# Performance work log

Hardware: AMD Instinct MI355X
Metric: run time of the kernel (lower is better)

## Reference

```python
import jax, jax.numpy as jnp
import numpy as np

NORM_S = 3.0  # normalize_scale, learn_scale=False
NUM_CLASSES = 32


def setup_inputs() -> dict:
    key = jax.random.key(0)
    k1, k2 = jax.random.split(key)
    x = jax.random.normal(k1, (512, 128), dtype=jnp.float32)
    labels = jax.random.randint(k2, (512,), 0, NUM_CLASSES, dtype=jnp.int64)
    return {"x": x, "labels": labels}


def reference(x, labels):
    # L2-normalize rows and scale (MyTripletLoss.forward)
    f = NORM_S * x / jnp.linalg.norm(x, axis=1, keepdims=True)
    # pairwise squared distances, clamped at 0 (pairwise_distances)
    sq = jnp.sum(f * f, axis=1)
    D = jnp.clip(sq[:, None] + sq[None, :] - 2.0 * (f @ f.T), 0.0, None)  # [N,N]
    N = x.shape[0]
    # triplet_type == 0: valid triplet (i,j,k) iff i!=j, l_i==l_j, l_i!=l_k
    same = (labels[:, None] == labels[None, :]) & (~jnp.eye(N, dtype=bool))  # [i,j]
    diff = labels[:, None] != labels[None, :]                                # [i,k]
    mask = same[:, :, None] & diff[:, None, :]                               # [i,j,k]
    # DBL loss: log(1 + exp(D_ij - D_ik)) = softplus
    lt = jax.nn.softplus(D[:, :, None] - D[:, None, :])                      # [i,j,k]
    triplet_count = jnp.sum(mask).astype(lt.dtype)
    loss = jnp.sum(jnp.where(mask, lt, 0.0)) / triplet_count
    return loss.reshape(1)
```

## Files before the change

kernel.cpp:

```cpp
#include <hip/hip_runtime.h>
#include <math.h>

#define N 512
#define DIM 128
#define NORM_S 3.0f
#define TR 64
#define PADS 132


__global__ void __launch_bounds__(64) normalize_kernel(const float* __restrict__ x,
                                                       float* __restrict__ f) {
    int row = blockIdx.x;
    int lane = threadIdx.x;
    const float2* xr = (const float2*)(x + row * DIM);
    float2 v = xr[lane];
    float s = v.x * v.x + v.y * v.y;
    #pragma unroll
    for (int off = 32; off > 0; off >>= 1) s += __shfl_xor(s, off, 64);
    float scale = NORM_S / sqrtf(s);
    float2 fv;
    fv.x = v.x * scale;
    fv.y = v.y * scale;
    ((float2*)(f + row * DIM))[lane] = fv;
}

__global__ void __launch_bounds__(256) triplet_kernel(const float* __restrict__ f,
                                                      const int* __restrict__ labels,
                                                      float* __restrict__ sums,
                                                      float* __restrict__ cnts) {
    __shared__ float xt[TR * PADS];
    __shared__ float xi[DIM];
    __shared__ int   lab[N];
    __shared__ float sameD[N];
    __shared__ float diffD[N];
    __shared__ float part[256];
    __shared__ float red[256];
    __shared__ int   nsame, ndiff;

    int i = blockIdx.x;
    int t = threadIdx.x;

    if (t < DIM) xi[t] = f[i * DIM + t];
    for (int j = t; j < N; j += 256) lab[j] = labels[j];
    if (t == 0) { nsame = 0; ndiff = 0; }
    __syncthreads();

    int li = lab[i];
    int jloc  = t & (TR - 1);
    int quart = t >> 6;
    int dbase = quart * 32;

    float4 bx[8];
    {
        const float4* b = (const float4*)(xi + dbase);
        #pragma unroll
        for (int q = 0; q < 8; ++q) bx[q] = b[q];
    }

    for (int tile = 0; tile < N / TR; ++tile) {
        int base = tile * TR;
        const float4* src = (const float4*)(f + base * DIM);
        #pragma unroll
        for (int k = 0; k < (TR * DIM / 4) / 256; ++k) {
            int e  = t + k * 256;
            int r  = e >> 5;
            int c4 = e & 31;
            float4 v = src[e];
            *((float4*)(xt + r * PADS + 4 * c4)) = v;
        }
        __syncthreads();

        {
            const float4* a = (const float4*)(xt + jloc * PADS + dbase);
            float d0 = 0.0f, d1 = 0.0f;
            #pragma unroll
            for (int q = 0; q < 8; q += 2) {
                float4 a0 = a[q + 0];
                float4 a1 = a[q + 1];
                d0 += a0.x * bx[q].x + a0.y * bx[q].y + a0.z * bx[q].z + a0.w * bx[q].w;
                d1 += a1.x * bx[q + 1].x + a1.y * bx[q + 1].y + a1.z * bx[q + 1].z + a1.w * bx[q + 1].w;
            }
            part[t] = d0 + d1;
        }
        __syncthreads();

        if (t < TR) {
            float dot = part[t] + part[t + 64] + part[t + 128] + part[t + 192];
            int j = base + t;
            float D = fmaxf(0.0f, 18.0f - 2.0f * dot);
            int lj = lab[j];
            if (lj == li) {
                if (j != i) { int p = atomicAdd(&nsame, 1); sameD[p] = D; }
            } else {
                int p = atomicAdd(&ndiff, 1); diffD[p] = D;
            }
        }
        __syncthreads();
    }

    int ns = nsame, nd = ndiff;
    float lsum = 0.0f;
    for (int js = 0; js < ns; ++js) {
        float Dij = sameD[js];
        for (int ks = t; ks < nd; ks += 256) {
            float d = Dij - diffD[ks];
            lsum += __logf(1.0f + __expf(d));
        }
    }

    red[t] = lsum;
    __syncthreads();
    #pragma unroll
    for (int s = 128; s > 0; s >>= 1) {
        if (t < s) red[t] += red[t + s];
        __syncthreads();
    }
    if (t == 0) {
        sums[i] = red[0];
        cnts[i] = (float)(ns * nd);
    }
}

__global__ void __launch_bounds__(256) finalize_kernel(const float* __restrict__ sums,
                                                       const float* __restrict__ cnts,
                                                       float* __restrict__ out) {
    __shared__ float2 red[256];
    int t = threadIdx.x;
    float2 v;
    v.x = sums[t] + sums[t + 256];
    v.y = cnts[t] + cnts[t + 256];
    red[t] = v;
    __syncthreads();
    #pragma unroll
    for (int s = 128; s > 0; s >>= 1) {
        if (t < s) {
            red[t].x += red[t + s].x;
            red[t].y += red[t + s].y;
        }
        __syncthreads();
    }
    if (t == 0) out[0] = red[0].x / red[0].y;
}

extern "C" void kernel_launch(void* const* d_in, const int* in_sizes, int n_in,
                              void* d_out, int out_size, void* d_ws, size_t ws_size,
                              hipStream_t stream) {
    const float* x      = (const float*)d_in[0];
    const int*   labels = (const int*)d_in[1];
    float*       out    = (float*)d_out;

    float* f    = (float*)d_ws;
    float* sums = f + N * DIM;
    float* cnts = sums + N;

    normalize_kernel<<<N, 64, 0, stream>>>(x, f);
    triplet_kernel<<<N, 256, 0, stream>>>(f, labels, sums, cnts);
    finalize_kernel<<<1, 256, 0, stream>>>(sums, cnts, out);
}
```

Measured before the change: 74.18 us.

## Fuse normalize and finalize into a single cooperative triplet kernel

Drops the separate normalization kernel: each block computes its own row's inverse norm and, inside the tiled dot-product loop, the squared norms of the other rows, so distances come straight from raw x. The final reduction moves into the same kernel behind a grid-wide cooperative sync, so three launches become one. In exchange the norm work is recomputed in every block, and the grid sync requires all 512 blocks to be co-resident and adds a grid barrier.

After: 144.1 us. 94.3% more time.

```diff
diff --git a/kernel.cpp b/kernel.cpp
--- a/kernel.cpp
+++ b/kernel.cpp
@@ -1,5 +1,8 @@
 #include <hip/hip_runtime.h>
+#include <hip/hip_cooperative_groups.h>
 #include <math.h>
+
+namespace cg = cooperative_groups;
 
 #define N 512
 #define DIM 128
@@ -7,45 +10,43 @@
 #define TR 64
 #define PADS 132
 
-
-__global__ void __launch_bounds__(64) normalize_kernel(const float* __restrict__ x,
-                                                       float* __restrict__ f) {
-    int row = blockIdx.x;
-    int lane = threadIdx.x;
-    const float2* xr = (const float2*)(x + row * DIM);
-    float2 v = xr[lane];
-    float s = v.x * v.x + v.y * v.y;
-    #pragma unroll
-    for (int off = 32; off > 0; off >>= 1) s += __shfl_xor(s, off, 64);
-    float scale = NORM_S / sqrtf(s);
-    float2 fv;
-    fv.x = v.x * scale;
-    fv.y = v.y * scale;
-    ((float2*)(f + row * DIM))[lane] = fv;
-}
-
-__global__ void __launch_bounds__(256) triplet_kernel(const float* __restrict__ f,
+__global__ void __launch_bounds__(256) triplet_kernel(const float* __restrict__ x,
                                                       const int* __restrict__ labels,
                                                       float* __restrict__ sums,
-                                                      float* __restrict__ cnts) {
+                                                      float* __restrict__ cnts,
+                                                      float* __restrict__ out) {
     __shared__ float xt[TR * PADS];
     __shared__ float xi[DIM];
     __shared__ int   lab[N];
     __shared__ float sameD[N];
     __shared__ float diffD[N];
-    __shared__ float part[256];
+    __shared__ float partd[256];
+    __shared__ float parts[256];
     __shared__ float red[256];
+    __shared__ float red2[256];
+    __shared__ float rni_sh;
     __shared__ int   nsame, ndiff;
 
     int i = blockIdx.x;
     int t = threadIdx.x;
 
-    if (t < DIM) xi[t] = f[i * DIM + t];
+    if (t < DIM) xi[t] = x[i * DIM + t];
     for (int j = t; j < N; j += 256) lab[j] = labels[j];
     if (t == 0) { nsame = 0; ndiff = 0; }
     __syncthreads();
 
-    int li = lab[i];
+    red[t] = (t < DIM) ? xi[t] * xi[t] : 0.0f;
+    __syncthreads();
+    #pragma unroll
+    for (int s = 128; s > 0; s >>= 1) {
+        if (t < s) red[t] += red[t + s];
+        __syncthreads();
+    }
+    if (t == 0) rni_sh = rsqrtf(red[0]);
+    __syncthreads();
+
+    int li  = lab[i];
+    float rni = rni_sh;
     int jloc  = t & (TR - 1);
     int quart = t >> 6;
     int dbase = quart * 32;
@@ -59,7 +60,7 @@
 
     for (int tile = 0; tile < N / TR; ++tile) {
         int base = tile * TR;
-        const float4* src = (const float4*)(f + base * DIM);
+        const float4* src = (const float4*)(x + base * DIM);
         #pragma unroll
         for (int k = 0; k < (TR * DIM / 4) / 256; ++k) {
             int e  = t + k * 256;
@@ -72,22 +73,27 @@
 
         {
             const float4* a = (const float4*)(xt + jloc * PADS + dbase);
-            float d0 = 0.0f, d1 = 0.0f;
+            float d0 = 0.0f, d1 = 0.0f, s0 = 0.0f, s1 = 0.0f;
             #pragma unroll
             for (int q = 0; q < 8; q += 2) {
                 float4 a0 = a[q + 0];
                 float4 a1 = a[q + 1];
                 d0 += a0.x * bx[q].x + a0.y * bx[q].y + a0.z * bx[q].z + a0.w * bx[q].w;
                 d1 += a1.x * bx[q + 1].x + a1.y * bx[q + 1].y + a1.z * bx[q + 1].z + a1.w * bx[q + 1].w;
+                s0 += a0.x * a0.x + a0.y * a0.y + a0.z * a0.z + a0.w * a0.w;
+                s1 += a1.x * a1.x + a1.y * a1.y + a1.z * a1.z + a1.w * a1.w;
             }
-            part[t] = d0 + d1;
+            partd[t] = d0 + d1;
+            parts[t] = s0 + s1;
         }
         __syncthreads();
 
         if (t < TR) {
-            float dot = part[t] + part[t + 64] + part[t + 128] + part[t + 192];
+            float dot = partd[t] + partd[t + 64] + partd[t + 128] + partd[t + 192];
+            float ss  = parts[t] + parts[t + 64] + parts[t + 128] + parts[t + 192];
+            float rnj = rsqrtf(ss);
             int j = base + t;
-            float D = fmaxf(0.0f, 18.0f - 2.0f * dot);
+            float D = 18.0f * fmaxf(0.0f, 1.0f - dot * rni * rnj);
             int lj = lab[j];
             if (lj == li) {
                 if (j != i) { int p = atomicAdd(&nsame, 1); sameD[p] = D; }
@@ -119,27 +125,26 @@
         sums[i] = red[0];
         cnts[i] = (float)(ns * nd);
     }
-}
+    __threadfence();
 
-__global__ void __launch_bounds__(256) finalize_kernel(const float* __restrict__ sums,
-                                                       const float* __restrict__ cnts,
-                                                       float* __restrict__ out) {
-    __shared__ float2 red[256];
-    int t = threadIdx.x;
-    float2 v;
-    v.x = sums[t] + sums[t + 256];
-    v.y = cnts[t] + cnts[t + 256];
-    red[t] = v;
-    __syncthreads();
-    #pragma unroll
-    for (int s = 128; s > 0; s >>= 1) {
-        if (t < s) {
-            red[t].x += red[t + s].x;
-            red[t].y += red[t + s].y;
+    cg::this_grid().sync();
+
+    if (i == 0) {
+        float sv = sums[t] + sums[t + 256];
+        float cv = cnts[t] + cnts[t + 256];
+        red[t]  = sv;
+        red2[t] = cv;
+        __syncthreads();
+        #pragma unroll
+        for (int s = 128; s > 0; s >>= 1) {
+            if (t < s) {
+                red[t]  += red[t + s];
+                red2[t] += red2[t + s];
+            }
+            __syncthreads();
         }
-        __syncthreads();
+        if (t == 0) out[0] = red[0] / red2[0];
     }
-    if (t == 0) out[0] = red[0].x / red[0].y;
 }
 
 extern "C" void kernel_launch(void* const* d_in, const int* in_sizes, int n_in,
@@ -149,11 +154,10 @@
     const int*   labels = (const int*)d_in[1];
     float*       out    = (float*)d_out;
 
-    float* f    = (float*)d_ws;
-    float* sums = f + N * DIM;
+    float* sums = (float*)d_ws;
     float* cnts = sums + N;
 
-    normalize_kernel<<<N, 64, 0, stream>>>(x, f);
-    triplet_kernel<<<N, 256, 0, stream>>>(f, labels, sums, cnts);
-    finalize_kernel<<<1, 256, 0, stream>>>(sums, cnts, out);
+    void* args[] = {(void*)&x, (void*)&labels, (void*)&sums, (void*)&cnts, (void*)&out};
+    hipLaunchCooperativeKernel((const void*)triplet_kernel,
+                               dim3(N), dim3(256), args, 0, stream);
 }
```
